# Performance work log

Hardware: AMD Instinct MI355X
Metric: run time of the kernel (lower is better)

Reference implementation:

```python
import jax, jax.numpy as jnp
import numpy as np

N = 40000   # nodes
E = 150000  # edges (before self-loops)
G = 128     # graphs in batch
V = 20000   # vocab
D = 512     # embedding/hidden dim
H = 4       # heads (layers 0,1)
C = 128     # per-head channels (H*C = D)


def setup_inputs() -> dict:
    key = jax.random.key(0)
    ks = jax.random.split(key, 64)
    n = lambda i, shp, s=0.05: jax.random.normal(ks[i], shp, dtype=jnp.float32) * s
    inp = {}
    inp['node_ids'] = jax.random.randint(ks[0], (N,), 0, V, dtype=jnp.int32)
    inp['edge_index'] = jax.random.randint(ks[1], (2, E), 0, N, dtype=jnp.int32)
    inp['batch'] = jnp.sort(jax.random.randint(ks[2], (N,), 0, G, dtype=jnp.int32))
    inp['emb'] = n(3, (V, D), 0.02)
    # GAT layer 0: D -> H x C, concat
    inp['W0'] = n(4, (D, H * C)); inp['as0'] = n(5, (H, C)); inp['ad0'] = n(6, (H, C)); inp['b0'] = n(7, (D,), 0.01)
    # GAT layer 1: D -> H x C, concat
    inp['W1'] = n(8, (D, H * C)); inp['as1'] = n(9, (H, C)); inp['ad1'] = n(10, (H, C)); inp['b1'] = n(11, (D,), 0.01)
    inp['W2'] = n(12, (D, D)); inp['as2'] = n(13, (1, D)); inp['ad2'] = n(14, (1, D)); inp['b2'] = n(15, (D,), 0.01)
    # danger head
    inp['dW1'] = n(16, (D, D)); inp['db1'] = n(17, (D,), 0.01)
    inp['dg1'] = 1.0 + n(18, (D,), 0.02); inp['dbt1'] = n(19, (D,), 0.02)
    inp['drm1'] = n(20, (D,), 0.02); inp['drv1'] = jax.random.uniform(ks[21], (D,)) + 0.5
    inp['dW2'] = n(22, (D, D // 2)); inp['db2'] = n(23, (D // 2,), 0.01)
    inp['dg2'] = 1.0 + n(24, (D // 2,), 0.02); inp['dbt2'] = n(25, (D // 2,), 0.02)
    inp['drm2'] = n(26, (D // 2,), 0.02); inp['drv2'] = jax.random.uniform(ks[27], (D // 2,)) + 0.5
    inp['dW3'] = n(28, (D // 2, 1)); inp['db3'] = n(29, (1,), 0.01)
    # synergy head
    inp['sW1'] = n(30, (D, D)); inp['sb1'] = n(31, (D,), 0.01)
    inp['sg1'] = 1.0 + n(32, (D,), 0.02); inp['sbt1'] = n(33, (D,), 0.02)
    inp['srm1'] = n(34, (D,), 0.02); inp['srv1'] = jax.random.uniform(ks[35], (D,)) + 0.5
    inp['sW2'] = n(36, (D, D // 2)); inp['sb2'] = n(37, (D // 2,), 0.01)
    inp['sg2'] = 1.0 + n(38, (D // 2,), 0.02); inp['sbt2'] = n(39, (D // 2,), 0.02)
    inp['srm2'] = n(40, (D // 2,), 0.02); inp['srv2'] = jax.random.uniform(ks[41], (D // 2,)) + 0.5
    inp['sW3'] = n(42, (D // 2, 1)); inp['sb3'] = n(43, (1,), 0.01)
    return inp


def _gat(x, W, a_src, a_dst, bias, src, dst, heads, ch, concat):
    # PyG GATConv (eval): linear, per-head additive attention, softmax over
    # incoming edges per destination node, scatter-add aggregate.
    n_nodes = x.shape[0]
    h = (x @ W).reshape(n_nodes, heads, ch)              # [N,H,C]
    e_s = jnp.sum(h * a_src, axis=-1)                    # [N,H]
    e_d = jnp.sum(h * a_dst, axis=-1)                    # [N,H]
    e = jax.nn.leaky_relu(e_s[src] + e_d[dst], 0.2)      # [E,H]
    m = jax.ops.segment_max(e, dst, num_segments=n_nodes)
    m = jnp.where(jnp.isfinite(m), m, 0.0)
    p = jnp.exp(e - m[dst])
    s = jax.ops.segment_sum(p, dst, num_segments=n_nodes)
    alpha = p / (s[dst] + 1e-16)                         # [E,H]
    out = jax.ops.segment_sum(h[src] * alpha[:, :, None], dst, num_segments=n_nodes)
    out = out.reshape(n_nodes, heads * ch) if concat else out.mean(axis=1)
    return out + bias


def _bn(x, g, b, rm, rv):
    return (x - rm) * jax.lax.rsqrt(rv + 1e-5) * g + b


def _head(p, W1, b1, g1, bt1, rm1, rv1, W2, b2, g2, bt2, rm2, rv2, W3, b3):
    z = jax.nn.relu(_bn(p @ W1 + b1, g1, bt1, rm1, rv1))
    z = jax.nn.relu(_bn(z @ W2 + b2, g2, bt2, rm2, rv2))
    return jax.nn.sigmoid(z @ W3 + b3)


def reference(node_ids, edge_index, batch, emb, W0, as0, ad0, b0, W1, as1, ad1, b1, W2, as2, ad2, b2, dW1, db1, dg1, dbt1, drm1, drv1, dW2, db2, dg2, dbt2, drm2, drv2, dW3, db3, sW1, sb1, sg1, sbt1, srm1, srv1, sW2, sb2, sg2, sbt2, srm2, srv2, sW3, sb3):
    loops = jnp.arange(N, dtype=edge_index.dtype)
    src = jnp.concatenate([edge_index[0], loops])
    dst = jnp.concatenate([edge_index[1], loops])
    x = emb[node_ids]                                    # [N,D]
    # layer 0 (no residual)
    x = jax.nn.relu(_gat(x, W0, as0, ad0, b0, src, dst, H, C, True))
    # layer 1 (+residual)
    x = x + jax.nn.relu(_gat(x, W1, as1, ad1, b1, src, dst, H, C, True))
    # layer 2 (+residual)
    x = x + jax.nn.relu(_gat(x, W2, as2, ad2, b2, src, dst, 1, D, False))
    # global mean pool per graph
    sums = jax.ops.segment_sum(x, batch, num_segments=G)
    cnt = jax.ops.segment_sum(jnp.ones((N,), x.dtype), batch, num_segments=G)
    pooled = sums / jnp.maximum(cnt, 1.0)[:, None]       # [G,D]
    danger = _head(pooled, dW1, db1, dg1, dbt1, drm1, drv1, dW2, db2, dg2, dbt2, drm2, drv2, dW3, db3)
    synergy = _head(pooled, sW1, sb1, sg1, sbt1, srm1, srv1, sW2, sb2, sg2, sbt2, srm2, srv2, sW3, sb3)
    return danger, synergy
```

## Files before the change

### kernel.cpp

```cpp
#include <hip/hip_runtime.h>
#include <hip/hip_bf16.h>
#include <stdint.h>

#define NN 40000
#define EE 150000
#define ET 190000
#define GG 128
#define DD 512
#define MP 40064
#define GNB 1252
#define GNBF 1248
#define WB 192
#define NPB 20000
#define FB 743
#define CW 32
#define NB8 5000

typedef __hip_bfloat16 bf16;
typedef __attribute__((ext_vector_type(8))) short s16x8;
typedef __attribute__((ext_vector_type(4))) float f32v4;

__device__ __forceinline__ float b2f(bf16 v) { return __bfloat162float(v); }
__device__ __forceinline__ bf16  f2b(float v) { return __float2bfloat16(v); }
__device__ __forceinline__ unsigned f2bu(float v) {
    bf16 b = __float2bfloat16(v);
    return (unsigned)*(unsigned short*)&b;
}
__device__ __forceinline__ float lo16(unsigned u) { return __uint_as_float(u << 16); }
__device__ __forceinline__ float hi16(unsigned u) { return __uint_as_float(u & 0xffff0000u); }
__device__ __forceinline__ float s2f(short s) {
    return __uint_as_float(((unsigned)(unsigned short)s) << 16);
}

__device__ __forceinline__ void gl_lds16(const void* g, void* l) {
    __builtin_amdgcn_global_load_lds(
        (const __attribute__((address_space(1))) unsigned int*)g,
        (__attribute__((address_space(3))) unsigned int*)l, 16, 0, 0);
}

__global__ __launch_bounds__(256) void k_prep(const float* __restrict__ W0,
                                              const float* __restrict__ W1,
                                              const float* __restrict__ W2,
                                              bf16* __restrict__ Wt0,
                                              bf16* __restrict__ Wt1,
                                              bf16* __restrict__ Wt2,
                                              const int* __restrict__ ids,
                                              const float4* __restrict__ emb4,
                                              bf16* __restrict__ xb,
                                              const int* __restrict__ esrc,
                                              const int* __restrict__ edst,
                                              int* __restrict__ deg,
                                              int* __restrict__ csrf) {
    __shared__ float tile[64][65];
    int b = blockIdx.x, tid = threadIdx.x;
    if (b < WB) {
        int wi = b >> 6, tl = b & 63;
        const float* W; bf16* Wt;
        if (wi == 0)      { W = W0; Wt = Wt0; }
        else if (wi == 1) { W = W1; Wt = Wt1; }
        else              { W = W2; Wt = Wt2; }
        int n0 = (tl & 7) * 64, k0 = (tl >> 3) * 64;
        int rr = tid >> 4, cc = (tid & 15) * 4;
        #pragma unroll
        for (int i = 0; i < 4; i++) {
            int k = k0 + i * 16 + rr;
            float4 v = *(const float4*)(W + (size_t)k * DD + n0 + cc);
            tile[cc + 0][i * 16 + rr] = v.x;
            tile[cc + 1][i * 16 + rr] = v.y;
            tile[cc + 2][i * 16 + rr] = v.z;
            tile[cc + 3][i * 16 + rr] = v.w;
        }
        __syncthreads();
        #pragma unroll
        for (int i = 0; i < 4; i++) {
            int nl = i * 16 + rr;
            ushort4 o;
            o.x = (unsigned short)f2bu(tile[nl][cc + 0]);
            o.y = (unsigned short)f2bu(tile[nl][cc + 1]);
            o.z = (unsigned short)f2bu(tile[nl][cc + 2]);
            o.w = (unsigned short)f2bu(tile[nl][cc + 3]);
            *(ushort4*)(Wt + (size_t)(n0 + nl) * DD + k0 + cc) = o;
        }
    } else if (b < WB + NPB) {
        int t = (b - WB) * 256 + tid;
        int n = t >> 7, c = t & 127;
        if (n >= NN) return;
        int id = ids[n];
        float4 v = emb4[(size_t)id * 128 + c];
        ushort4 u;
        u.x = (unsigned short)f2bu(v.x); u.y = (unsigned short)f2bu(v.y);
        u.z = (unsigned short)f2bu(v.z); u.w = (unsigned short)f2bu(v.w);
        *(ushort4*)(xb + (size_t)n * DD + c * 4) = u;
    } else {
        int e = (b - WB - NPB) * 256 + tid;
        if (e >= ET) return;
        int dst, src;
        if (e < EE) { dst = edst[e]; src = esrc[e]; }
        else        { dst = e - EE;  src = dst; }
        int slot = atomicAdd(&deg[dst], 1);
        if (slot < CW) csrf[dst * CW + slot] = src;
    }
}

template <int H>
__global__ __launch_bounds__(512) void k_gemm_mfma(const bf16* __restrict__ A,
                                                   const bf16* __restrict__ Bt,
                                                   bf16* __restrict__ C,
                                                   const float* __restrict__ a_s,
                                                   const float* __restrict__ a_d,
                                                   float* __restrict__ es,
                                                   float* __restrict__ ed) {
    constexpr int K = DD, N = DD;
    __shared__ bf16 smem[4 * 128 * 64];
    bf16* lA0 = smem;
    bf16* lB0 = smem + 8192;
    bf16* lA1 = smem + 16384;
    bf16* lB1 = smem + 24576;
    int tid = threadIdx.x, lane = tid & 63, quad = lane >> 4, l16 = lane & 15;
    int w = tid >> 6;

    int bid = blockIdx.x, mt, nt;
    if (bid >= GNBF) { mt = MP / 128 - 1; nt = bid - GNBF; }
    else { nt = (bid & 31) >> 3; mt = (bid >> 5) * 8 + (bid & 7); }
    int m0 = mt * 128, n0 = nt * 128;
    int wm = (w & 1) * 64, wn = (w >> 1) * 32;

    int l8 = lane >> 3, c16 = (lane & 7) << 4;
    int scol = c16 ^ (l8 << 4);
    const char* pAg = (const char*)A + (size_t)(m0 + w * 16 + l8) * (K * 2) + scol;
    const char* pBg = (const char*)Bt + (size_t)(n0 + w * 16 + l8) * (K * 2) + scol;
    char* dA0 = (char*)lA0 + w * 2048;
    char* dB0 = (char*)lB0 + w * 2048;
    char* dA1 = (char*)lA1 + w * 2048;
    char* dB1 = (char*)lB1 + w * 2048;

    int aoff[2][4], boff[2][2];
    #pragma unroll
    for (int kk = 0; kk < 2; kk++) {
        #pragma unroll
        for (int i = 0; i < 4; i++) {
            int qb = (kk * 4 + quad) << 4;
            int rowA = wm + i * 16 + l16;
            aoff[kk][i] = rowA * 64 + ((qb ^ ((rowA & 7) << 4)) >> 1);
        }
        #pragma unroll
        for (int j = 0; j < 2; j++) {
            int qb = (kk * 4 + quad) << 4;
            int rowB = wn + j * 16 + l16;
            boff[kk][j] = rowB * 64 + ((qb ^ ((rowB & 7) << 4)) >> 1);
        }
    }

    f32v4 zero = 0;
    f32v4 acc[4][2];
    #pragma unroll
    for (int i = 0; i < 4; i++)
        #pragma unroll
        for (int j = 0; j < 2; j++) acc[i][j] = zero;

    auto stage = [&](int kb, char* dA, char* dB) {
        #pragma unroll
        for (int i = 0; i < 2; i++) {
            gl_lds16(pAg + i * 8192 + kb, dA + i * 1024);
            gl_lds16(pBg + i * 8192 + kb, dB + i * 1024);
        }
    };
    auto compute = [&](const bf16* bA, const bf16* bB) {
        #pragma unroll
        for (int kk = 0; kk < 2; kk++) {
            s16x8 a[4], b[2];
            #pragma unroll
            for (int i = 0; i < 4; i++) a[i] = *(const s16x8*)(bA + aoff[kk][i]);
            #pragma unroll
            for (int j = 0; j < 2; j++) b[j] = *(const s16x8*)(bB + boff[kk][j]);
            #pragma unroll
            for (int i = 0; i < 4; i++)
                #pragma unroll
                for (int j = 0; j < 2; j++)
                    acc[i][j] = __builtin_amdgcn_mfma_f32_16x16x32_bf16(a[i], b[j], acc[i][j], 0, 0, 0);
        }
    };

    stage(0, dA0, dB0);
    __syncthreads();
    #pragma unroll
    for (int k0 = 0; k0 < K; k0 += 128) {
        stage((k0 + 64) * 2, dA1, dB1);
        compute(lA0, lB0);
        __syncthreads();
        if (k0 + 128 < K) stage((k0 + 128) * 2, dA0, dB0);
        compute(lA1, lB1);
        __syncthreads();
    }

    float* asl = (float*)(smem + 8192);
    float* adl = asl + 128;
    if (tid < 128)       asl[tid] = a_s[n0 + tid];
    else if (tid < 256)  adl[tid - 128] = a_d[n0 + tid - 128];

    constexpr int ESTR = 136;
    bf16* ebuf = smem;
    int lrB = (w & 1) * 16 + quad * 4;
    int lr = tid >> 4, cc8 = (tid & 15) * 8;
    int grow = m0 + (lr >> 4) * 64 + (lr & 15);
    #pragma unroll
    for (int i = 0; i < 4; i++) {
        __syncthreads();
        #pragma unroll
        for (int j = 0; j < 2; j++) {
            int col = wn + j * 16 + l16;
            #pragma unroll
            for (int r = 0; r < 4; r++)
                ebuf[(lrB + r) * ESTR + col] = f2b(acc[i][j][r]);
        }
        __syncthreads();
        s16x8 v0 = *(s16x8*)(ebuf + lr * ESTR + cc8);
        float ses = 0.f, sed = 0.f;
        #pragma unroll
        for (int k = 0; k < 8; k++) {
            float x = s2f(v0[k]);
            ses += x * asl[cc8 + k];
            sed += x * adl[cc8 + k];
        }
        #pragma unroll
        for (int off = 1; off < 16; off <<= 1) {
            ses += __shfl_xor(ses, off, 64);
            sed += __shfl_xor(sed, off, 64);
        }
        int row = grow + i * 16;
        if ((tid & 15) == 0) {
            if (H == 4) {
                es[(size_t)row * 4 + nt] = ses;
                ed[(size_t)row * 4 + nt] = sed;
            } else {
                es[(size_t)nt * MP + row] = ses;
                ed[(size_t)nt * MP + row] = sed;
            }
        }
        *(s16x8*)(C + (size_t)row * N + n0 + cc8) = v0;
    }
}

template <int H, bool RES, bool FUSE>
__global__ __launch_bounds__(256) void k_gat_aggregate(const bf16* __restrict__ h,
                                                       const float* __restrict__ es,
                                                       const float* __restrict__ ed,
                                                       const int* __restrict__ degv,
                                                       const int* __restrict__ csrf,
                                                       const float* __restrict__ bias,
                                                       bf16* __restrict__ xb,
                                                       const int* __restrict__ batch,
                                                       float* __restrict__ psum,
                                                       float* __restrict__ pp) {
    __shared__ int   s_src[8][32];
    __shared__ float s_a[8][32 * H];
    __shared__ int   s_deg[8];
    __shared__ int   s_gb[FUSE ? 8 : 1];
    __shared__ int   s_g0;
    __shared__ float s_acc[FUSE ? 4 : 1][FUSE ? 8 : 1][FUSE ? 64 : 1];
    int tid = threadIdx.x, w = tid >> 6, lane = tid & 63;
    int half = lane >> 5, el = lane & 31;
    int nb = blockIdx.x * 8;
    if (FUSE && tid == 0) s_g0 = batch[nb];
    {
        int ln = w * 2 + half;
        int node = nb + ln;
        int deg = degv[node];
        if (deg > CW) deg = CW;
        if (el == 0) {
            s_deg[ln] = deg;
            if (FUSE) s_gb[ln] = batch[node];
        }
        float edl[H];
        if (H == 4) {
            #pragma unroll
            for (int hh = 0; hh < H; hh++) edl[hh] = ed[node * H + hh];
        } else {
            edl[0] = ed[node] + ed[MP + node] + ed[2 * MP + node] + ed[3 * MP + node];
        }
        float e_h[H];
        #pragma unroll
        for (int hh = 0; hh < H; hh++) e_h[hh] = -1e30f;
        if (el < deg) {
            int src = csrf[node * CW + el];
            s_src[ln][el] = src;
            if (H == 4) {
                float4 e4 = *(const float4*)(es + (size_t)src * 4);
                float t4[4] = {e4.x, e4.y, e4.z, e4.w};
                #pragma unroll
                for (int hh = 0; hh < 4; hh++) {
                    float e = t4[hh] + edl[hh];
                    e_h[hh] = e > 0.f ? e : 0.2f * e;
                }
            } else {
                float esv = es[src] + es[MP + src] + es[2 * MP + src] + es[3 * MP + src];
                float e = esv + edl[0];
                e_h[0] = e > 0.f ? e : 0.2f * e;
            }
        }
        float m[H];
        #pragma unroll
        for (int hh = 0; hh < H; hh++) m[hh] = e_h[hh];
        #pragma unroll
        for (int off = 16; off; off >>= 1)
            #pragma unroll
            for (int hh = 0; hh < H; hh++) m[hh] = fmaxf(m[hh], __shfl_xor(m[hh], off, 64));
        float p[H], sum[H];
        #pragma unroll
        for (int hh = 0; hh < H; hh++) {
            p[hh] = (el < deg) ? __expf(e_h[hh] - m[hh]) : 0.f;
            sum[hh] = p[hh];
        }
        #pragma unroll
        for (int off = 16; off; off >>= 1)
            #pragma unroll
            for (int hh = 0; hh < H; hh++) sum[hh] += __shfl_xor(sum[hh], off, 64);
        if (el < deg)
            #pragma unroll
            for (int hh = 0; hh < H; hh++) s_a[ln][el * H + hh] = p[hh] / (sum[hh] + 1e-16f);
    }
    __syncthreads();

    int dbase = lane * 8;
    int hd = (H == 4) ? (lane >> 4) : 0;
    float4 bi0 = *(const float4*)(bias + dbase);
    float4 bi1 = *(const float4*)(bias + dbase + 4);
    int ln0 = w * 2, ln1 = w * 2 + 1;
    int deg0 = s_deg[ln0], deg1 = s_deg[ln1];
    int dmax = deg0 > deg1 ? deg0 : deg1;
    if (FUSE) {
        #pragma unroll
        for (int k = 0; k < 8; k++) s_acc[w][k][lane] = 0.f;
    }
    float A0[8] = {}, A1[8] = {};
    for (int i = 0; i < dmax; i++) {
        if (i < deg0) {
            uint4 u = *(const uint4*)(h + (size_t)s_src[ln0][i] * DD + dbase);
            float a = s_a[ln0][i * H + hd];
            A0[0] += a * lo16(u.x); A0[1] += a * hi16(u.x);
            A0[2] += a * lo16(u.y); A0[3] += a * hi16(u.y);
            A0[4] += a * lo16(u.z); A0[5] += a * hi16(u.z);
            A0[6] += a * lo16(u.w); A0[7] += a * hi16(u.w);
        }
        if (i < deg1) {
            uint4 u = *(const uint4*)(h + (size_t)s_src[ln1][i] * DD + dbase);
            float a = s_a[ln1][i * H + hd];
            A1[0] += a * lo16(u.x); A1[1] += a * hi16(u.x);
            A1[2] += a * lo16(u.y); A1[3] += a * hi16(u.y);
            A1[4] += a * lo16(u.z); A1[5] += a * hi16(u.z);
            A1[6] += a * lo16(u.w); A1[7] += a * hi16(u.w);
        }
    }
    #pragma unroll
    for (int t = 0; t < 2; t++) {
        float* A = (t == 0) ? A0 : A1;
        int nn = w * 2 + t;
        float v[8];
        v[0] = A[0] + bi0.x; v[1] = A[1] + bi0.y;
        v[2] = A[2] + bi0.z; v[3] = A[3] + bi0.w;
        v[4] = A[4] + bi1.x; v[5] = A[5] + bi1.y;
        v[6] = A[6] + bi1.z; v[7] = A[7] + bi1.w;
        #pragma unroll
        for (int k = 0; k < 8; k++) v[k] = fmaxf(v[k], 0.f);
        size_t base = (size_t)(nb + nn) * DD + dbase;
        if (RES) {
            uint4 u = *(const uint4*)(xb + base);
            v[0] += lo16(u.x); v[1] += hi16(u.x);
            v[2] += lo16(u.y); v[3] += hi16(u.y);
            v[4] += lo16(u.z); v[5] += hi16(u.z);
            v[6] += lo16(u.w); v[7] += hi16(u.w);
        }
        if (FUSE) {
            int gn = s_gb[nn];
            if (gn == s_g0) {
                #pragma unroll
                for (int k = 0; k < 8; k++) s_acc[w][k][lane] += v[k];
            } else {
                #pragma unroll
                for (int k = 0; k < 8; k++)
                    atomicAdd(&psum[(size_t)gn * DD + dbase + k], v[k]);
            }
        } else {
            uint4 o;
            o.x = f2bu(v[0]) | (f2bu(v[1]) << 16);
            o.y = f2bu(v[2]) | (f2bu(v[3]) << 16);
            o.z = f2bu(v[4]) | (f2bu(v[5]) << 16);
            o.w = f2bu(v[6]) | (f2bu(v[7]) << 16);
            *(uint4*)(xb + base) = o;
        }
    }
    if (FUSE) {
        __syncthreads();
        int d = tid << 1;
        float a0 = s_acc[0][d & 7][d >> 3] + s_acc[1][d & 7][d >> 3]
                 + s_acc[2][d & 7][d >> 3] + s_acc[3][d & 7][d >> 3];
        int d1 = d + 1;
        float a1 = s_acc[0][d1 & 7][d1 >> 3] + s_acc[1][d1 & 7][d1 >> 3]
                 + s_acc[2][d1 & 7][d1 >> 3] + s_acc[3][d1 & 7][d1 >> 3];
        float2 o = {a0, a1};
        *(float2*)(pp + (size_t)blockIdx.x * DD + d) = o;
    }
}

__global__ __launch_bounds__(256) void k_pool_red(const int* __restrict__ batch,
                                                  const float* __restrict__ pp,
                                                  float* __restrict__ psum) {
    int g = blockIdx.x;
    __shared__ int s_lo, s_hi;
    if (threadIdx.x == 0) {
        int lo = 0, hi = NB8;
        while (lo < hi) { int mid = (lo + hi) >> 1; if (batch[mid * 8] < g) lo = mid + 1; else hi = mid; }
        s_lo = lo;
        lo = 0; hi = NB8;
        while (lo < hi) { int mid = (lo + hi) >> 1; if (batch[mid * 8] < g + 1) lo = mid + 1; else hi = mid; }
        s_hi = lo;
    }
    __syncthreads();
    int d = threadIdx.x * 2;
    float a0 = 0.f, a1 = 0.f;
    for (int b = s_lo; b < s_hi; b++) {
        float2 v = *(const float2*)(pp + (size_t)b * DD + d);
        a0 += v.x; a1 += v.y;
    }
    psum[(size_t)g * DD + d]     += a0;
    psum[(size_t)g * DD + d + 1] += a1;
}

template <int Din, int Dout, bool FIRST>
__global__ __launch_bounds__(256) void k_head_layer2(const float* __restrict__ inD,
                                                     const float* __restrict__ inS,
                                                     const int* __restrict__ batch,
                                                     const float* __restrict__ Wd, const float* __restrict__ bd,
                                                     const float* __restrict__ gd, const float* __restrict__ btd,
                                                     const float* __restrict__ rmd, const float* __restrict__ rvd,
                                                     const float* __restrict__ Ws, const float* __restrict__ bs_,
                                                     const float* __restrict__ gs, const float* __restrict__ bts,
                                                     const float* __restrict__ rms, const float* __restrict__ rvs,
                                                     float* __restrict__ outD,
                                                     float* __restrict__ outS) {
    const float *in, *W, *b, *ga, *bt, *rm, *rv; float* out;
    if (blockIdx.z == 0) { in = inD; W = Wd; b = bd; ga = gd; bt = btd; rm = rmd; rv = rvd; out = outD; }
    else                 { in = inS; W = Ws; b = bs_; ga = gs; bt = bts; rm = rms; rv = rvs; out = outS; }
    int g = blockIdx.y;
    int tid = threadIdx.x;
    int j = blockIdx.x * 64 + (tid & 63);
    int ks = tid >> 6;
    __shared__ float s_in[Din];
    __shared__ float s_red[256];
    __shared__ float s_inv;
    if (FIRST) {
        if (tid == 0) {
            int lo = 0, hi = NN;
            while (lo < hi) { int mid = (lo + hi) >> 1; if (batch[mid] < g) lo = mid + 1; else hi = mid; }
            int a = lo; lo = 0; hi = NN;
            while (lo < hi) { int mid = (lo + hi) >> 1; if (batch[mid] < g + 1) lo = mid + 1; else hi = mid; }
            s_inv = 1.f / fmaxf((float)(lo - a), 1.f);
        }
        __syncthreads();
        for (int k = tid; k < Din; k += 256) s_in[k] = in[(size_t)g * DD + k] * s_inv;
    } else {
        for (int k = tid; k < Din; k += 256) s_in[k] = in[(size_t)g * Din + k];
    }
    __syncthreads();
    constexpr int KS = Din / 4;
    const float* Wp = W + (size_t)ks * KS * Dout + j;
    float acc = 0.f;
    #pragma unroll 8
    for (int k = 0; k < KS; k++) acc += s_in[ks * KS + k] * Wp[(size_t)k * Dout];
    s_red[tid] = acc;
    __syncthreads();
    if (tid < 64) {
        float s = s_red[tid] + s_red[tid + 64] + s_red[tid + 128] + s_red[tid + 192];
        s += b[j];
        s = (s - rm[j]) * rsqrtf(rv[j] + 1e-5f) * ga[j] + bt[j];
        out[(size_t)g * Dout + j] = s > 0.f ? s : 0.f;
    }
}

__global__ __launch_bounds__(64) void k_head_final2(const float* __restrict__ zD,
                                                    const float* __restrict__ zS,
                                                    const float* __restrict__ W3d, const float* __restrict__ b3d,
                                                    const float* __restrict__ W3s, const float* __restrict__ b3s,
                                                    float* __restrict__ out, int Din) {
    const float* z; const float* W3; const float* b3; float* o;
    if (blockIdx.y == 0) { z = zD; W3 = W3d; b3 = b3d; o = out; }
    else                 { z = zS; W3 = W3s; b3 = b3s; o = out + GG; }
    int g = blockIdx.x, lane = threadIdx.x;
    float s = 0.f;
    for (int k = lane; k < Din; k += 64) s += z[(size_t)g * Din + k] * W3[k];
    #pragma unroll
    for (int off = 32; off; off >>= 1) s += __shfl_xor(s, off, 64);
    if (lane == 0) {
        s += b3[0];
        o[g] = 1.f / (1.f + __expf(-s));
    }
}

extern "C" void kernel_launch(void* const* d_in, const int* in_sizes, int n_in,
                              void* d_out, int out_size, void* d_ws, size_t ws_size,
                              hipStream_t stream) {
    const int*   node_ids = (const int*)d_in[0];
    const int*   ei       = (const int*)d_in[1];
    const int*   batch    = (const int*)d_in[2];
    const float* emb      = (const float*)d_in[3];
    const float* W0  = (const float*)d_in[4],  *as0 = (const float*)d_in[5];
    const float* ad0 = (const float*)d_in[6],  *b0  = (const float*)d_in[7];
    const float* W1  = (const float*)d_in[8],  *as1 = (const float*)d_in[9];
    const float* ad1 = (const float*)d_in[10], *b1  = (const float*)d_in[11];
    const float* W2  = (const float*)d_in[12], *as2 = (const float*)d_in[13];
    const float* ad2 = (const float*)d_in[14], *b2  = (const float*)d_in[15];
    const float* dW1 = (const float*)d_in[16], *db1 = (const float*)d_in[17];
    const float* dg1 = (const float*)d_in[18], *dbt1= (const float*)d_in[19];
    const float* drm1= (const float*)d_in[20], *drv1= (const float*)d_in[21];
    const float* dW2 = (const float*)d_in[22], *db2 = (const float*)d_in[23];
    const float* dg2 = (const float*)d_in[24], *dbt2= (const float*)d_in[25];
    const float* drm2= (const float*)d_in[26], *drv2= (const float*)d_in[27];
    const float* dW3 = (const float*)d_in[28], *db3 = (const float*)d_in[29];
    const float* sW1 = (const float*)d_in[30], *sb1 = (const float*)d_in[31];
    const float* sg1 = (const float*)d_in[32], *sbt1= (const float*)d_in[33];
    const float* srm1= (const float*)d_in[34], *srv1= (const float*)d_in[35];
    const float* sW2 = (const float*)d_in[36], *sb2 = (const float*)d_in[37];
    const float* sg2 = (const float*)d_in[38], *sbt2= (const float*)d_in[39];
    const float* srm2= (const float*)d_in[40], *srv2= (const float*)d_in[41];
    const float* sW3 = (const float*)d_in[42], *sb3 = (const float*)d_in[43];

    const int* esrc = ei;
    const int* edst = ei + EE;

    char* p = (char*)d_ws;
    auto alloc = [&](size_t bytes) { char* r = p; p += (bytes + 255) & ~(size_t)255; return (void*)r; };
    bf16*  xb      = (bf16*)alloc((size_t)MP * DD * 2);
    bf16*  hbuf    = (bf16*)alloc((size_t)MP * DD * 2);
    bf16*  Wt0     = (bf16*)alloc((size_t)DD * DD * 2);
    bf16*  Wt1     = (bf16*)alloc((size_t)DD * DD * 2);
    bf16*  Wt2     = (bf16*)alloc((size_t)DD * DD * 2);
    float* esed    = (float*)alloc((size_t)6 * MP * 4 * 4);
    float* es0 = esed,              *ed0 = esed + (size_t)MP * 4;
    float* es1 = esed + (size_t)MP * 8,  *ed1 = esed + (size_t)MP * 12;
    float* es2 = esed + (size_t)MP * 16, *ed2 = esed + (size_t)MP * 20;
    int*   deg     = (int*)alloc((size_t)NN * 4);
    int*   csrf    = (int*)alloc((size_t)NN * CW * 4);
    float* psum    = (float*)alloc((size_t)GG * DD * 4);
    float* pp      = (float*)alloc((size_t)NB8 * DD * 4);
    float* z1d     = (float*)alloc((size_t)GG * DD * 4);
    float* z1s     = (float*)alloc((size_t)GG * DD * 4);
    float* z2d     = (float*)alloc((size_t)GG * 256 * 4);
    float* z2s     = (float*)alloc((size_t)GG * 256 * 4);

    hipMemsetAsync(deg, 0, (size_t)NN * 4, stream);
    hipMemsetAsync(psum, 0, (size_t)GG * DD * 4, stream);
    k_prep<<<WB + NPB + FB, 256, 0, stream>>>(W0, W1, W2, Wt0, Wt1, Wt2,
                                              node_ids, (const float4*)emb, xb,
                                              esrc, edst, deg, csrf);

    k_gemm_mfma<4><<<GNB, 512, 0, stream>>>(xb, Wt0, hbuf, as0, ad0, es0, ed0);
    k_gat_aggregate<4, false, false><<<NB8, 256, 0, stream>>>(hbuf, es0, ed0, deg, csrf, b0, xb, nullptr, nullptr, nullptr);

    k_gemm_mfma<4><<<GNB, 512, 0, stream>>>(xb, Wt1, hbuf, as1, ad1, es1, ed1);
    k_gat_aggregate<4, true, false><<<NB8, 256, 0, stream>>>(hbuf, es1, ed1, deg, csrf, b1, xb, nullptr, nullptr, nullptr);

    k_gemm_mfma<1><<<GNB, 512, 0, stream>>>(xb, Wt2, hbuf, as2, ad2, es2, ed2);
    k_gat_aggregate<1, true, true><<<NB8, 256, 0, stream>>>(hbuf, es2, ed2, deg, csrf, b2, xb, batch, psum, pp);
    k_pool_red<<<GG, 256, 0, stream>>>(batch, pp, psum);

    float* outp = (float*)d_out;
    dim3 h1grid(DD / 64, GG, 2);
    k_head_layer2<DD, DD, true><<<h1grid, 256, 0, stream>>>(psum, psum, batch,
        dW1, db1, dg1, dbt1, drm1, drv1,
        sW1, sb1, sg1, sbt1, srm1, srv1, z1d, z1s);
    dim3 h2grid(256 / 64, GG, 2);
    k_head_layer2<DD, 256, false><<<h2grid, 256, 0, stream>>>(z1d, z1s, batch,
        dW2, db2, dg2, dbt2, drm2, drv2,
        sW2, sb2, sg2, sbt2, srm2, srv2, z2d, z2s);
    dim3 fgrid(GG, 2);
    k_head_final2<<<fgrid, 64, 0, stream>>>(z2d, z2s, dW3, db3, sW3, sb3, outp, 256);
}
```

Before: 454.2 us.

## Apply layer-0 projection to vocabulary table and gather projected rows in aggregation

Instead of gathering embeddings per node and multiplying 40000 rows by W0, the first GEMM multiplies the (padded) 20000-row embedding table by W0. The layer-0 aggregation then remaps node and source indices through node_ids to fetch projected features and attention logits. This halves the first GEMM and the embedding conversion. In exchange, the aggregation adds an extra indirection and more scattered reads.

```diff
diff --git a/kernel.cpp b/kernel.cpp
--- a/kernel.cpp
+++ b/kernel.cpp
@@ -7,11 +7,11 @@
 #define ET 190000
 #define GG 128
 #define DD 512
+#define VV 20000
+#define VP 20480
 #define MP 40064
-#define GNB 1252
-#define GNBF 1248
 #define WB 192
-#define NPB 20000
+#define NPB0 10240
 #define FB 743
 #define CW 32
 #define NB8 5000
@@ -44,9 +44,8 @@
                                               bf16* __restrict__ Wt0,
                                               bf16* __restrict__ Wt1,
                                               bf16* __restrict__ Wt2,
-                                              const int* __restrict__ ids,
                                               const float4* __restrict__ emb4,
-                                              bf16* __restrict__ xb,
+                                              bf16* __restrict__ embb,
                                               const int* __restrict__ esrc,
                                               const int* __restrict__ edst,
                                               int* __restrict__ deg,
@@ -81,18 +80,18 @@
             o.w = (unsigned short)f2bu(tile[nl][cc + 3]);
             *(ushort4*)(Wt + (size_t)(n0 + nl) * DD + k0 + cc) = o;
         }
-    } else if (b < WB + NPB) {
+    } else if (b < WB + NPB0) {
         int t = (b - WB) * 256 + tid;
-        int n = t >> 7, c = t & 127;
-        if (n >= NN) return;
-        int id = ids[n];
-        float4 v = emb4[(size_t)id * 128 + c];
+        int v = t >> 7, c = t & 127;
         ushort4 u;
-        u.x = (unsigned short)f2bu(v.x); u.y = (unsigned short)f2bu(v.y);
-        u.z = (unsigned short)f2bu(v.z); u.w = (unsigned short)f2bu(v.w);
-        *(ushort4*)(xb + (size_t)n * DD + c * 4) = u;
+        if (v < VV) {
+            float4 x = emb4[(size_t)v * 128 + c];
+            u.x = (unsigned short)f2bu(x.x); u.y = (unsigned short)f2bu(x.y);
+            u.z = (unsigned short)f2bu(x.z); u.w = (unsigned short)f2bu(x.w);
+        } else { u.x = 0; u.y = 0; u.z = 0; u.w = 0; }
+        *(ushort4*)(embb + (size_t)v * DD + c * 4) = u;
     } else {
-        int e = (b - WB - NPB) * 256 + tid;
+        int e = (b - WB - NPB0) * 256 + tid;
         if (e >= ET) return;
         int dst, src;
         if (e < EE) { dst = edst[e]; src = esrc[e]; }
@@ -102,7 +101,7 @@
     }
 }
 
-template <int H>
+template <int H, int MT>
 __global__ __launch_bounds__(512) void k_gemm_mfma(const bf16* __restrict__ A,
                                                    const bf16* __restrict__ Bt,
                                                    bf16* __restrict__ C,
@@ -111,6 +110,7 @@
                                                    float* __restrict__ es,
                                                    float* __restrict__ ed) {
     constexpr int K = DD, N = DD;
+    constexpr int GNBFk = (MT / 8) * 32;
     __shared__ bf16 smem[4 * 128 * 64];
     bf16* lA0 = smem;
     bf16* lB0 = smem + 8192;
@@ -120,7 +120,7 @@
     int w = tid >> 6;
 
     int bid = blockIdx.x, mt, nt;
-    if (bid >= GNBF) { mt = MP / 128 - 1; nt = bid - GNBF; }
+    if (bid >= GNBFk) { int r = bid - GNBFk; mt = (MT & ~7) + (r >> 2); nt = r & 3; }
     else { nt = (bid & 31) >> 3; mt = (bid >> 5) * 8 + (bid & 7); }
     int m0 = mt * 128, n0 = nt * 128;
     int wm = (w & 1) * 64, wn = (w >> 1) * 32;
@@ -241,7 +241,7 @@
     }
 }
 
-template <int H, bool RES, bool FUSE>
+template <int H, bool RES, bool FUSE, bool GI>
 __global__ __launch_bounds__(256) void k_gat_aggregate(const bf16* __restrict__ h,
                                                        const float* __restrict__ es,
                                                        const float* __restrict__ ed,
@@ -251,7 +251,8 @@
                                                        bf16* __restrict__ xb,
                                                        const int* __restrict__ batch,
                                                        float* __restrict__ psum,
-                                                       float* __restrict__ pp) {
+                                                       float* __restrict__ pp,
+                                                       const int* __restrict__ idsmap) {
     __shared__ int   s_src[8][32];
     __shared__ float s_a[8][32 * H];
     __shared__ int   s_deg[8];
@@ -273,8 +274,9 @@
         }
         float edl[H];
         if (H == 4) {
-            #pragma unroll
-            for (int hh = 0; hh < H; hh++) edl[hh] = ed[node * H + hh];
+            int nd = GI ? idsmap[node] : node;
+            #pragma unroll
+            for (int hh = 0; hh < H; hh++) edl[hh] = ed[nd * H + hh];
         } else {
             edl[0] = ed[node] + ed[MP + node] + ed[2 * MP + node] + ed[3 * MP + node];
         }
@@ -283,6 +285,7 @@
         for (int hh = 0; hh < H; hh++) e_h[hh] = -1e30f;
         if (el < deg) {
             int src = csrf[node * CW + el];
+            if (GI) src = idsmap[src];
             s_src[ln][el] = src;
             if (H == 4) {
                 float4 e4 = *(const float4*)(es + (size_t)src * 4);
@@ -531,6 +534,7 @@
     auto alloc = [&](size_t bytes) { char* r = p; p += (bytes + 255) & ~(size_t)255; return (void*)r; };
     bf16*  xb      = (bf16*)alloc((size_t)MP * DD * 2);
     bf16*  hbuf    = (bf16*)alloc((size_t)MP * DD * 2);
+    bf16*  embb    = (bf16*)alloc((size_t)VP * DD * 2);
     bf16*  Wt0     = (bf16*)alloc((size_t)DD * DD * 2);
     bf16*  Wt1     = (bf16*)alloc((size_t)DD * DD * 2);
     bf16*  Wt2     = (bf16*)alloc((size_t)DD * DD * 2);
@@ -549,18 +553,18 @@
 
     hipMemsetAsync(deg, 0, (size_t)NN * 4, stream);
     hipMemsetAsync(psum, 0, (size_t)GG * DD * 4, stream);
-    k_prep<<<WB + NPB + FB, 256, 0, stream>>>(W0, W1, W2, Wt0, Wt1, Wt2,
-                                              node_ids, (const float4*)emb, xb,
-                                              esrc, edst, deg, csrf);
-
-    k_gemm_mfma<4><<<GNB, 512, 0, stream>>>(xb, Wt0, hbuf, as0, ad0, es0, ed0);
-    k_gat_aggregate<4, false, false><<<NB8, 256, 0, stream>>>(hbuf, es0, ed0, deg, csrf, b0, xb, nullptr, nullptr, nullptr);
-
-    k_gemm_mfma<4><<<GNB, 512, 0, stream>>>(xb, Wt1, hbuf, as1, ad1, es1, ed1);
-    k_gat_aggregate<4, true, false><<<NB8, 256, 0, stream>>>(hbuf, es1, ed1, deg, csrf, b1, xb, nullptr, nullptr, nullptr);
-
-    k_gemm_mfma<1><<<GNB, 512, 0, stream>>>(xb, Wt2, hbuf, as2, ad2, es2, ed2);
-    k_gat_aggregate<1, true, true><<<NB8, 256, 0, stream>>>(hbuf, es2, ed2, deg, csrf, b2, xb, batch, psum, pp);
+    k_prep<<<WB + NPB0 + FB, 256, 0, stream>>>(W0, W1, W2, Wt0, Wt1, Wt2,
+                                               (const float4*)emb, embb,
+                                               esrc, edst, deg, csrf);
+
+    k_gemm_mfma<4, VP / 128><<<(VP / 128) * 4, 512, 0, stream>>>(embb, Wt0, hbuf, as0, ad0, es0, ed0);
+    k_gat_aggregate<4, false, false, true><<<NB8, 256, 0, stream>>>(hbuf, es0, ed0, deg, csrf, b0, xb, nullptr, nullptr, nullptr, node_ids);
+
+    k_gemm_mfma<4, MP / 128><<<(MP / 128) * 4, 512, 0, stream>>>(xb, Wt1, hbuf, as1, ad1, es1, ed1);
+    k_gat_aggregate<4, true, false, false><<<NB8, 256, 0, stream>>>(hbuf, es1, ed1, deg, csrf, b1, xb, nullptr, nullptr, nullptr, nullptr);
+
+    k_gemm_mfma<1, MP / 128><<<(MP / 128) * 4, 512, 0, stream>>>(xb, Wt2, hbuf, as2, ad2, es2, ed2);
+    k_gat_aggregate<1, true, true, false><<<NB8, 256, 0, stream>>>(hbuf, es2, ed2, deg, csrf, b2, xb, batch, psum, pp, nullptr);
     k_pool_red<<<GG, 256, 0, stream>>>(batch, pp, psum);
 
     float* outp = (float*)d_out;
```

Result: faster. 441.3 us (-2.8%).
